# Performance work log

Hardware: AMD Instinct MI355X
Metric: run time of the kernel (lower is better)

The kernel has to match this reference:

```python
import jax, jax.numpy as jnp
import numpy as np

HIDDEN = 768

def setup_inputs() -> dict:
    key = jax.random.key(0)
    ks = jax.random.split(key, 7)
    x = jax.random.normal(ks[0], (4, 4096, HIDDEN), dtype=jnp.float32)
    s = 1.0 / np.sqrt(HIDDEN)
    Wq = jax.random.uniform(ks[1], (HIDDEN, HIDDEN), minval=-s, maxval=s, dtype=jnp.float32)
    Wk = jax.random.uniform(ks[2], (HIDDEN, HIDDEN), minval=-s, maxval=s, dtype=jnp.float32)
    Wv = jax.random.uniform(ks[3], (HIDDEN, HIDDEN), minval=-s, maxval=s, dtype=jnp.float32)
    bq = jax.random.uniform(ks[4], (HIDDEN,), minval=-s, maxval=s, dtype=jnp.float32)
    bk = jax.random.uniform(ks[5], (HIDDEN,), minval=-s, maxval=s, dtype=jnp.float32)
    bv = jax.random.uniform(ks[6], (HIDDEN,), minval=-s, maxval=s, dtype=jnp.float32)
    return {"x": x, "Wq": Wq, "bq": bq, "Wk": Wk, "bk": bk, "Wv": Wv, "bv": bv}

def reference(x, Wq, bq, Wk, bk, Wv, bv):
    # q,k,v: [b, s, d]
    q = jnp.einsum('bsd,de->bse', x, Wq.T) + bq
    k = jnp.einsum('bsd,de->bse', x, Wk.T) + bk
    v = jnp.einsum('bsd,de->bse', x, Wv.T) + bv
    scale = 1.0 / jnp.sqrt(jnp.asarray(x.shape[-1], dtype=x.dtype))
    scores = jnp.einsum('bqd,bkd->bqk', q, k) * scale  # [b, s, s]
    attn = jax.nn.softmax(scores, axis=-1)
    return jnp.einsum('bqk,bkd->bqd', attn, v)
```

## Files before the change

### kernel.cpp

```cpp
#include <hip/hip_runtime.h>
#include <stdint.h>

typedef unsigned short u16;
typedef __attribute__((ext_vector_type(8))) short    bf16x8;
typedef __attribute__((ext_vector_type(4))) float    f32x4;

__device__ __forceinline__ u16 f2bf(float f) {
    unsigned u = __float_as_uint(f);
    u = (u + 0x7fffu + ((u >> 16) & 1u)) >> 16;
    return (u16)u;
}

__global__ __launch_bounds__(256) void cast_all_kernel(const float* __restrict__ x,
                                                       const float* __restrict__ w0,
                                                       const float* __restrict__ w1,
                                                       const float* __restrict__ w2,
                                                       u16* __restrict__ xb,
                                                       u16* __restrict__ wb) {
    const int b = blockIdx.x;
    if (b < 12288) {
        int i = b * 256 + threadIdx.x;
        float4 f = ((const float4*)x)[i];
        ushort4 o;
        o.x = f2bf(f.x); o.y = f2bf(f.y); o.z = f2bf(f.z); o.w = f2bf(f.w);
        ((ushort4*)xb)[i] = o;
    } else {
        const int i2 = b - 12288;
        const int w  = i2 / 576;
        const int blk = i2 - w * 576;
        const float* src = (w == 0) ? w0 : (w == 1) ? w1 : w2;
        int i = blk * 256 + threadIdx.x;
        float4 f = ((const float4*)src)[i];
        ushort4 o;
        o.x = f2bf(f.x); o.y = f2bf(f.y); o.z = f2bf(f.z); o.w = f2bf(f.w);
        ((ushort4*)wb)[(size_t)w * 147456 + i] = o;
    }
}

__global__ __launch_bounds__(256) void transpose_bf16_kernel(const u16* __restrict__ V,
                                                             u16* __restrict__ Vt,
                                                             float* __restrict__ rsum) {
    __shared__ u16 tile[32][33];
    const int t = threadIdx.x;
    if (blockIdx.x == 0 && blockIdx.z == 0) {
        int idx = blockIdx.y * 256 + t;
        if (idx < 16384) rsum[idx] = 0.f;
    }
    const size_t z = blockIdx.z;
    const u16* Vb  = V  + z * (size_t)4096 * 2304;
    u16*       Vtb = Vt + z * (size_t)768 * 4096;
    const int c0 = blockIdx.x * 32;
    const int r0 = blockIdx.y * 32;
    const int lr = t >> 3;
    const int lc = (t & 7) * 4;
    ushort4 in = *(const ushort4*)&Vb[(size_t)(r0 + lr) * 2304 + c0 + lc];
    tile[lr][lc + 0] = in.x; tile[lr][lc + 1] = in.y;
    tile[lr][lc + 2] = in.z; tile[lr][lc + 3] = in.w;
    __syncthreads();
    ushort4 o;
    o.x = tile[lc + 0][lr]; o.y = tile[lc + 1][lr];
    o.z = tile[lc + 2][lr]; o.w = tile[lc + 3][lr];
    *(ushort4*)&Vtb[(size_t)(c0 + lr) * 4096 + r0 + lc] = o;
}

template <int EPI, int WN, int NBX, int GRP, int NGRID, int NBY, int MINW>
__global__ __launch_bounds__(256, MINW) void gemm_bt_kernel(
        const u16* __restrict__ A, const u16* __restrict__ B, void* __restrict__ Cv,
        const float* __restrict__ b0, const float* __restrict__ b1, const float* __restrict__ b2,
        float* __restrict__ rs, float s2, int K,
        int lda, int ldb, int ldc, long batchA, long batchB, long batchC) {
    __shared__ __align__(16) u16 As[128 * 64];
    __shared__ __align__(16) u16 Bs[32 * WN * 64];

    constexpr int SPX = NGRID / (8 * NBX);
    const int lin = blockIdx.x;
    const int c = lin & 7, p = lin >> 3;
    const int bxi = p % GRP;
    const int rest = p / GRP;
    const int s = rest % SPX;
    const int g = rest / SPX;
    const int bx = g * GRP + bxi;
    const int strip = c * SPX + s;
    const int by = strip % NBY;
    const int bz = strip / NBY;

    const int t = threadIdx.x;
    const long z = bz;
    const u16* Ab = A + z * batchA + (long)by * 128 * lda;
    const u16* Bb = B + z * batchB + (long)bx * (32 * WN) * ldb;

    const int lane = t & 63;
    const int wave = t >> 6;
    const int wm = wave >> 1, wn = wave & 1;
    const int quad = lane >> 4;
    const int frow = lane & 15;
    const int cc0 = quad ^ (frow & 7);

    f32x4 acc[4][WN];
#pragma unroll
    for (int i = 0; i < 4; i++)
#pragma unroll
        for (int j = 0; j < WN; j++)
#pragma unroll
            for (int e = 0; e < 4; e++) acc[i][j][e] = 0.f;

    int srow[WN], scol[WN];
#pragma unroll
    for (int j = 0; j < WN; j++) {
        const int d = t + j * 256;
        srow[j] = d >> 3;
        scol[j] = ((d & 7) ^ (srow[j] & 7)) * 8;
    }

    bf16x8 ra[4], rb[WN];
#pragma unroll
    for (int j = 0; j < 4; j++)
        ra[j] = *(const bf16x8*)(Ab + (long)srow[j] * lda + scol[j]);
#pragma unroll
    for (int j = 0; j < WN; j++)
        rb[j] = *(const bf16x8*)(Bb + (long)srow[j] * ldb + scol[j]);

    for (int kt = 0; kt < K; kt += 64) {
#pragma unroll
        for (int j = 0; j < 4; j++)
            *(bf16x8*)&As[(t + j * 256) * 8] = ra[j];
#pragma unroll
        for (int j = 0; j < WN; j++)
            *(bf16x8*)&Bs[(t + j * 256) * 8] = rb[j];
        __syncthreads();

        if (kt + 64 < K) {
            const int kn = kt + 64;
#pragma unroll
            for (int j = 0; j < 4; j++)
                ra[j] = *(const bf16x8*)(Ab + (long)srow[j] * lda + kn + scol[j]);
#pragma unroll
            for (int j = 0; j < WN; j++)
                rb[j] = *(const bf16x8*)(Bb + (long)srow[j] * ldb + kn + scol[j]);
        }

#pragma unroll
        for (int kk = 0; kk < 2; kk++) {
            const int cc = (cc0 ^ (kk * 4)) * 8;
            bf16x8 bfr[WN];
#pragma unroll
            for (int j = 0; j < WN; j++)
                bfr[j] = *(const bf16x8*)&Bs[(wn * WN * 16 + j * 16 + frow) * 64 + cc];
#pragma unroll
            for (int i = 0; i < 4; i++) {
                bf16x8 af = *(const bf16x8*)&As[(wm * 64 + i * 16 + frow) * 64 + cc];
#pragma unroll
                for (int j = 0; j < WN; j++)
                    acc[i][j] = __builtin_amdgcn_mfma_f32_16x16x32_bf16(af, bfr[j], acc[i][j], 0, 0, 0);
            }
        }
        __syncthreads();
    }

    const int m_base = by * 128 + wm * 64;
    const int n_base = bx * (32 * WN) + wn * (16 * WN);

    if (EPI == 0) {
        const int seg = n_base / 768;
        const float* bp = (seg == 0) ? b0 : (seg == 1) ? b1 : b2;
        u16* C = (u16*)Cv + z * batchC;
#pragma unroll
        for (int j = 0; j < WN; j++) {
            const int col = n_base + j * 16 + frow;
            const float bb = bp[col - seg * 768];
#pragma unroll
            for (int i = 0; i < 4; i++) {
                const int row0 = m_base + i * 16 + quad * 4;
#pragma unroll
                for (int r = 0; r < 4; r++)
                    C[(long)(row0 + r) * ldc + col] = f2bf(acc[i][j][r] + bb);
            }
        }
    } else if (EPI == 1) {
        u16* C = (u16*)Cv + z * batchC;
        float rowpart[4][4];
#pragma unroll
        for (int i = 0; i < 4; i++)
#pragma unroll
            for (int r = 0; r < 4; r++) rowpart[i][r] = 0.f;
#pragma unroll
        for (int i = 0; i < 4; i++) {
            const int row0 = m_base + i * 16 + quad * 4;
#pragma unroll
            for (int j = 0; j < WN; j++) {
                const int col = n_base + j * 16 + frow;
#pragma unroll
                for (int r = 0; r < 4; r++) {
                    float e = exp2f(acc[i][j][r] * s2);
                    C[(long)(row0 + r) * ldc + col] = f2bf(e);
                    rowpart[i][r] += e;
                }
            }
        }
#pragma unroll
        for (int i = 0; i < 4; i++)
#pragma unroll
            for (int r = 0; r < 4; r++) {
                float v = rowpart[i][r];
                v += __shfl_xor(v, 1); v += __shfl_xor(v, 2);
                v += __shfl_xor(v, 4); v += __shfl_xor(v, 8);
                if (frow == 0)
                    atomicAdd(&rs[z * 4096 + m_base + i * 16 + quad * 4 + r], v);
            }
    } else {
        float* C = (float*)Cv + z * batchC;
#pragma unroll
        for (int i = 0; i < 4; i++) {
            const int row0 = m_base + i * 16 + quad * 4;
            float inv[4];
#pragma unroll
            for (int r = 0; r < 4; r++) inv[r] = 1.0f / rs[z * 4096 + row0 + r];
#pragma unroll
            for (int j = 0; j < WN; j++) {
                const int col = n_base + j * 16 + frow;
#pragma unroll
                for (int r = 0; r < 4; r++)
                    C[(long)(row0 + r) * ldc + col] = acc[i][j][r] * inv[r];
            }
        }
    }
}

extern "C" void kernel_launch(void* const* d_in, const int* in_sizes, int n_in,
                              void* d_out, int out_size, void* d_ws, size_t ws_size,
                              hipStream_t stream) {
    const float* x  = (const float*)d_in[0];
    const float* Wq = (const float*)d_in[1];
    const float* bq = (const float*)d_in[2];
    const float* Wk = (const float*)d_in[3];
    const float* bk = (const float*)d_in[4];
    const float* Wv = (const float*)d_in[5];
    const float* bv = (const float*)d_in[6];
    float* out = (float*)d_out;

    uint8_t* ws = (uint8_t*)d_ws;
    u16*   xb   = (u16*)(ws + 0);
    u16*   Vt   = (u16*)(ws + 0);
    u16*   QKV  = (u16*)(ws + 25165824);
    u16*   E    = (u16*)(ws + 100663296);
    u16*   Wqkv = (u16*)(ws + 234881024);
    float* rsum = (float*)(ws + 234881024);

    cast_all_kernel<<<14016, 256, 0, stream>>>(x, Wq, Wk, Wv, xb, Wqkv);

    gemm_bt_kernel<0, 4, 18, 6, 2304, 128, 3><<<2304, 256, 0, stream>>>(
        xb, Wqkv, QKV, bq, bk, bv, nullptr, 0.f, 768, 768, 768, 2304, 0, 0, 0);

    transpose_bf16_kernel<<<dim3(24, 128, 4), 256, 0, stream>>>(QKV + 1536, Vt, rsum);

    gemm_bt_kernel<1, 8, 16, 4, 2048, 32, 2><<<2048, 256, 0, stream>>>(
        QKV, QKV + 768, E, nullptr, nullptr, nullptr, rsum, 0.05205954822032348f,
        768, 2304, 2304, 4096, (long)4096 * 2304, (long)4096 * 2304, (long)4096 * 4096);

    gemm_bt_kernel<2, 4, 6, 6, 768, 32, 3><<<768, 256, 0, stream>>>(
        E, Vt, out, nullptr, nullptr, nullptr, rsum, 0.f,
        4096, 4096, 4096, 768, (long)4096 * 4096, (long)768 * 4096, (long)4096 * 768);
}
```

Before: 409.5 us.

## Add dedicated QK^T score kernel with direct global-to-LDS loads and double buffering

Replaces the generic templated GEMM used for the QK^T + exp stage with a new 512-thread kernel. It streams A and B tiles straight into LDS with global_load_lds, double-buffers them, and reads them through swizzled ds_read_b128. It also adds XCD-aware block remapping and raises MFMA priority around the compute. The aim is to hide global-load latency and cut register staging for the largest GEMM, at the cost of hand-tuned waitcnt and barrier logic that could race if the counts are wrong.

Result: no change. 414.3 us (+1.2%).

```diff
diff --git a/kernel.cpp b/kernel.cpp
--- a/kernel.cpp
+++ b/kernel.cpp
@@ -10,6 +10,21 @@
     u = (u + 0x7fffu + ((u >> 16) & 1u)) >> 16;
     return (u16)u;
 }
+
+__device__ __forceinline__ void gload16(const u16* src, u16* dst) {
+    __builtin_amdgcn_global_load_lds((const __attribute__((address_space(1))) void*)src,
+                                     (__attribute__((address_space(3))) void*)dst,
+                                     16, 0, 0);
+}
+
+template <int IMM>
+__device__ __forceinline__ bf16x8 dsr128(uint32_t addr) {
+    bf16x8 r;
+    asm volatile("ds_read_b128 %0, %1 offset:%2" : "=v"(r) : "v"(addr), "i"(IMM));
+    return r;
+}
+
+#define LA(ARR) ((uint32_t)(uintptr_t)(__attribute__((address_space(3))) void*)&(ARR)[0])
 
 __global__ __launch_bounds__(256) void cast_all_kernel(const float* __restrict__ x,
                                                        const float* __restrict__ w0,
@@ -226,6 +241,143 @@
     }
 }
 
+template <int NBX, int NBY, int GRP, int NGRID>
+__global__ __launch_bounds__(512, 4) void gemm_tp_kernel(
+        const u16* __restrict__ A, const u16* __restrict__ B, u16* __restrict__ C,
+        float* __restrict__ rs, float s2, int K,
+        int lda, int ldb, int ldc, long batchA, long batchB, long batchC) {
+    __shared__ __align__(16) u16 As0[4096];
+    __shared__ __align__(16) u16 As1[4096];
+    __shared__ __align__(16) u16 Bs0[8192];
+    __shared__ __align__(16) u16 Bs1[8192];
+
+    constexpr int SPX = NGRID / (8 * NBX);
+    const int lin = blockIdx.x;
+    const int c = lin & 7, p = lin >> 3;
+    const int bxi = p % GRP;
+    const int rest = p / GRP;
+    const int s = rest % SPX;
+    const int g = rest / SPX;
+    const int bx = g * GRP + bxi;
+    const int strip = c * SPX + s;
+    const int by = strip % NBY;
+    const int bz = strip / NBY;
+
+    const int t = threadIdx.x;
+    const int lane = t & 63;
+    const int wave = t >> 6;
+    const int wm = wave >> 2, wn = wave & 3;
+    const int quad = lane >> 4, frow = lane & 15;
+
+    const u16* Ab = A + (long)bz * batchA + (long)by * 128 * lda;
+    const u16* Bb = B + (long)bz * batchB + (long)bx * 256 * ldb;
+
+    const int srow = ((t >> 3) << 1) | ((t >> 2) & 1);
+    const int scol = ((t & 3) ^ ((t >> 3) & 3)) * 8;
+
+    const uint32_t rdo2 = (uint32_t)(((frow >> 1) * 64
+                        + ((frow & 1) * 4 + (quad ^ ((frow >> 1) & 3))) * 8) * 2);
+    const uint32_t aof2 = (uint32_t)(wm * 2048 * 2) + rdo2;
+    const uint32_t bof2 = (uint32_t)(wn * 2048 * 2) + rdo2;
+
+    f32x4 acc[4][4];
+#pragma unroll
+    for (int i = 0; i < 4; i++)
+#pragma unroll
+        for (int j = 0; j < 4; j++)
+#pragma unroll
+            for (int e = 0; e < 4; e++) acc[i][j][e] = 0.f;
+
+    auto SA = [&](u16* dst, int kofs) {
+        gload16(Ab + (long)srow * lda + kofs + scol, dst + wave * 512);
+    };
+    auto SB = [&](u16* dst, int kofs) {
+        gload16(Bb + (long)srow * ldb + kofs + scol, dst + wave * 512);
+        gload16(Bb + (long)(srow + 128) * ldb + kofs + scol, dst + wave * 512 + 4096);
+    };
+
+    SA(As0, 0);  SB(Bs0, 0);
+    SA(As1, 32); SB(Bs1, 32);
+
+#define MFMA16(AF, BF)                                                           \
+    __builtin_amdgcn_s_setprio(1);                                               \
+    _Pragma("unroll")                                                            \
+    for (int i = 0; i < 4; ++i)                                                  \
+        _Pragma("unroll")                                                        \
+        for (int j = 0; j < 4; ++j)                                              \
+            acc[i][j] = __builtin_amdgcn_mfma_f32_16x16x32_bf16(                 \
+                AF[i], BF[j], acc[i][j], 0, 0, 0);                               \
+    __builtin_amdgcn_s_setprio(0);
+
+    for (int kt = 0; kt < K; kt += 64) {
+        const bool pre = (kt + 64 < K);
+        bf16x8 af[4], bf[4];
+
+        asm volatile("s_waitcnt vmcnt(3)" ::: "memory");
+        __builtin_amdgcn_s_barrier();
+        {
+            const uint32_t aAd = LA(As0) + aof2;
+            const uint32_t aBd = LA(Bs0) + bof2;
+            af[0] = dsr128<0>(aAd);    af[1] = dsr128<1024>(aAd);
+            af[2] = dsr128<2048>(aAd); af[3] = dsr128<3072>(aAd);
+            bf[0] = dsr128<0>(aBd);    bf[1] = dsr128<1024>(aBd);
+            bf[2] = dsr128<2048>(aBd); bf[3] = dsr128<3072>(aBd);
+        }
+        asm volatile("s_waitcnt lgkmcnt(0)" ::: "memory");
+        __builtin_amdgcn_sched_barrier(0);
+        __builtin_amdgcn_s_barrier();
+        if (pre) { SA(As0, kt + 64); SB(Bs0, kt + 64); }
+        __builtin_amdgcn_sched_barrier(0);
+        MFMA16(af, bf)
+
+        if (pre) asm volatile("s_waitcnt vmcnt(3)" ::: "memory");
+        else     asm volatile("s_waitcnt vmcnt(0)" ::: "memory");
+        __builtin_amdgcn_s_barrier();
+        {
+            const uint32_t aAd = LA(As1) + aof2;
+            const uint32_t aBd = LA(Bs1) + bof2;
+            af[0] = dsr128<0>(aAd);    af[1] = dsr128<1024>(aAd);
+            af[2] = dsr128<2048>(aAd); af[3] = dsr128<3072>(aAd);
+            bf[0] = dsr128<0>(aBd);    bf[1] = dsr128<1024>(aBd);
+            bf[2] = dsr128<2048>(aBd); bf[3] = dsr128<3072>(aBd);
+        }
+        asm volatile("s_waitcnt lgkmcnt(0)" ::: "memory");
+        __builtin_amdgcn_sched_barrier(0);
+        __builtin_amdgcn_s_barrier();
+        if (pre) { SA(As1, kt + 96); SB(Bs1, kt + 96); }
+        __builtin_amdgcn_sched_barrier(0);
+        MFMA16(af, bf)
+    }
+#undef MFMA16
+
+    const int m_base = by * 128 + wm * 64;
+    const int n_base = bx * 256 + wn * 64;
+    const long z = bz;
+    u16* Cb = C + z * batchC;
+#pragma unroll
+    for (int i = 0; i < 4; ++i) {
+        const int row0 = m_base + i * 16 + quad * 4;
+        float rp[4] = {0.f, 0.f, 0.f, 0.f};
+#pragma unroll
+        for (int j = 0; j < 4; ++j) {
+            const int col = n_base + j * 16 + frow;
+#pragma unroll
+            for (int r = 0; r < 4; ++r) {
+                float e = exp2f(acc[i][j][r] * s2);
+                Cb[(long)(row0 + r) * ldc + col] = f2bf(e);
+                rp[r] += e;
+            }
+        }
+#pragma unroll
+        for (int r = 0; r < 4; ++r) {
+            float v = rp[r];
+            v += __shfl_xor(v, 1); v += __shfl_xor(v, 2);
+            v += __shfl_xor(v, 4); v += __shfl_xor(v, 8);
+            if (frow == 0) atomicAdd(&rs[z * 4096 + row0 + r], v);
+        }
+    }
+}
+
 extern "C" void kernel_launch(void* const* d_in, const int* in_sizes, int n_in,
                               void* d_out, int out_size, void* d_ws, size_t ws_size,
                               hipStream_t stream) {
@@ -253,9 +405,9 @@
 
     transpose_bf16_kernel<<<dim3(24, 128, 4), 256, 0, stream>>>(QKV + 1536, Vt, rsum);
 
-    gemm_bt_kernel<1, 8, 16, 4, 2048, 32, 2><<<2048, 256, 0, stream>>>(
-        QKV, QKV + 768, E, nullptr, nullptr, nullptr, rsum, 0.05205954822032348f,
-        768, 2304, 2304, 4096, (long)4096 * 2304, (long)4096 * 2304, (long)4096 * 4096);
+    gemm_tp_kernel<16, 32, 4, 2048><<<2048, 512, 0, stream>>>(
+        QKV, QKV + 768, E, rsum, 0.05205954822032348f, 768,
+        2304, 2304, 4096, (long)4096 * 2304, (long)4096 * 2304, (long)4096 * 4096);
 
     gemm_bt_kernel<2, 4, 6, 6, 768, 32, 3><<<768, 256, 0, stream>>>(
         E, Vt, out, nullptr, nullptr, nullptr, rsum, 0.f,
```
